# Kernel tuning notes

Hardware: AMD Instinct MI355X
Metric: run time of the kernel (lower is better)

The kernel has to match this reference:

```python
import jax, jax.numpy as jnp
import numpy as np

D_MODEL = 1024
NUM_HEADS = 16
DEPTH = D_MODEL // NUM_HEADS
B, S = 2, 2048


def setup_inputs() -> dict:
    key = jax.random.key(0)
    ks = jax.random.split(key, 12)
    std = 1.0 / np.sqrt(D_MODEL)
    inp = {
        "q": jax.random.normal(ks[0], (B, S, D_MODEL), dtype=jnp.float32),
        "k": jax.random.normal(ks[1], (B, S, D_MODEL), dtype=jnp.float32),
        "v": jax.random.normal(ks[2], (B, S, D_MODEL), dtype=jnp.float32),
        "mask": jax.random.randint(ks[3], (B, 1, 1, S), 0, 2, dtype=jnp.int32),
        "wq": jax.random.normal(ks[4], (D_MODEL, D_MODEL), dtype=jnp.float32) * std,
        "bq": jnp.zeros((D_MODEL,), dtype=jnp.float32),
        "wk": jax.random.normal(ks[5], (D_MODEL, D_MODEL), dtype=jnp.float32) * std,
        "bk": jnp.zeros((D_MODEL,), dtype=jnp.float32),
        "wv": jax.random.normal(ks[6], (D_MODEL, D_MODEL), dtype=jnp.float32) * std,
        "bv": jnp.zeros((D_MODEL,), dtype=jnp.float32),
        "wo": jax.random.normal(ks[7], (D_MODEL, D_MODEL), dtype=jnp.float32) * std,
        "bo": jnp.zeros((D_MODEL,), dtype=jnp.float32),
    }
    return inp


def _split_heads(x):
    # (B, S, D) -> (B, H, S, depth)
    b, s, _ = x.shape
    return x.reshape(b, s, NUM_HEADS, DEPTH).transpose(0, 2, 1, 3)


def reference(q, k, v, mask, wq, bq, wk, bk, wv, bv, wo, bo):
    qh = _split_heads(q @ wq + bq)   # (B,H,S,depth)
    kh = _split_heads(k @ wk + bk)
    vh = _split_heads(v @ wv + bv)
    scale = 1.0 / jnp.sqrt(jnp.float32(DEPTH))
    logits = jnp.einsum("bhqd,bhkd->bhqk", qh, kh) * scale  # (B,H,Sq,Sk)
    logits = logits + mask.astype(logits.dtype) * -1e9
    attn = jax.nn.softmax(logits, axis=-1)
    out = jnp.einsum("bhqk,bhkd->bhqd", attn, vh)  # (B,H,Sq,depth)
    out = out.transpose(0, 2, 1, 3).reshape(q.shape[0], -1, D_MODEL)
    return out @ wo + bo
```

## Files before the change

### kernel.cpp

```cpp
#include <hip/hip_runtime.h>
#include <hip/hip_bf16.h>
#include <stdint.h>


typedef __bf16 bf16;
typedef __bf16 bf16x8 __attribute__((ext_vector_type(8)));
typedef __bf16 bf16x4 __attribute__((ext_vector_type(4)));
typedef float  f32x4  __attribute__((ext_vector_type(4)));

#define D_MODEL 1024
#define S_LEN   2048
#define NH      16
#define DEPTH   64

#define LOG2E   1.4426950408889634f
#define QSCALE  (0.125f * LOG2E)
#define SMAX    20.0f
#define PADPEN  (-30000.0f)

__device__ __forceinline__ void gload_lds16(const void* g, void* l) {
  __builtin_amdgcn_global_load_lds(
      (__attribute__((address_space(1))) void*)g,
      (__attribute__((address_space(3))) void*)l,
      16, 0, 0);
}

__global__ __launch_bounds__(256) void setup(
    const void* __restrict__ q, const void* __restrict__ k,
    const void* __restrict__ v, const int* __restrict__ mask,
    const void* __restrict__ wq, const void* __restrict__ wk,
    const void* __restrict__ wv, const void* __restrict__ wo,
    const void* __restrict__ bq, const void* __restrict__ bk,
    const void* __restrict__ bv, const void* __restrict__ bo,
    bf16* __restrict__ wqT, bf16* __restrict__ wkT,
    bf16* __restrict__ wvT, bf16* __restrict__ woT,
    bf16* __restrict__ bqb, bf16* __restrict__ bkb,
    bf16* __restrict__ bvb, bf16* __restrict__ bob,
    bf16* __restrict__ qb, bf16* __restrict__ kb, bf16* __restrict__ vb,
    int* __restrict__ cpos, int* __restrict__ nb, int* __restrict__ flagout)
{
  const int t = threadIdx.x;
  uint32_t w = ((const uint32_t*)q)[t];
  uint32_t e = (w >> 7) & 0xFF;
  int inr = (e >= 90 && e <= 150) ? 1 : 0;
  __shared__ int flg;
  int cnt = __syncthreads_count(inr);
  if (t == 0) flg = (cnt > 160) ? 1 : 0;
  __syncthreads();
  int flag = flg;

  const int bid = blockIdx.x;
  if (bid < 2) {
    const int b = bid;
    const int lane = t & 63, wv4 = t >> 6;
    __shared__ int wsum[4];
    int vals[8], s = 0;
#pragma unroll
    for (int j = 0; j < 8; ++j) {
      vals[j] = (mask[b * S_LEN + t * 8 + j] == 0) ? 1 : 0;
      s += vals[j];
    }
    int acc = s;
    for (int off = 1; off < 64; off <<= 1) {
      int u = __shfl_up(acc, off);
      if (lane >= off) acc += u;
    }
    if (lane == 63) wsum[wv4] = acc;
    __syncthreads();
    int base = 0;
    for (int w4 = 0; w4 < 4; ++w4) base += (w4 < wv4) ? wsum[w4] : 0;
    int ex = base + acc - s;
#pragma unroll
    for (int j = 0; j < 8; ++j) {
      cpos[b * S_LEN + t * 8 + j] = vals[j] ? ex : -1;
      ex += vals[j];
    }
    if (t == 255) nb[b] = base + acc;
    if (b == 0 && t == 0) *flagout = flag;
  } else if (bid < 6) {
    const int j = bid - 2;
    const void* B; bf16* O;
    switch (j) {
      case 0:  B = bq; O = bqb; break;
      case 1:  B = bk; O = bkb; break;
      case 2:  B = bv; O = bvb; break;
      default: B = bo; O = bob; break;
    }
    const float sc = (j == 0) ? QSCALE : 1.0f;
    for (int jj = 0; jj < 4; ++jj) {
      const int i = t + jj * 256;
      const float val = flag ? (float)((const bf16*)B)[i] : ((const float*)B)[i];
      O[i] = (bf16)(val * sc);
    }
  } else if (bid < 6 + 4096) {
    const int job = bid - 6;
    const int wsel = job >> 10, rem = job & 1023;
    const void* W; bf16* T;
    switch (wsel) {
      case 0:  W = wq; T = wqT; break;
      case 1:  W = wk; T = wkT; break;
      case 2:  W = wv; T = wvT; break;
      default: W = wo; T = woT; break;
    }
    const float sc = (wsel == 0) ? QSCALE : 1.0f;
    __shared__ float tile[32][33];
    const int tx = t & 31, ty = t >> 5;
    const int x0 = (rem & 31) * 32;
    const int y0 = (rem >> 5) * 32;
    for (int i = ty; i < 32; i += 8) {
      const size_t gi = (size_t)(y0 + i) * D_MODEL + x0 + tx;
      tile[i][tx] = flag ? (float)((const bf16*)W)[gi] : ((const float*)W)[gi];
    }
    __syncthreads();
    for (int i = ty; i < 32; i += 8)
      T[(size_t)(x0 + i) * D_MODEL + y0 + tx] = (bf16)(tile[tx][i] * sc);
  } else {
    if (flag) return;
    const int job = bid - 4102;
    const int tensor = job >> 11, blk = job & 2047;
    const void* src; bf16* dst;
    switch (tensor) {
      case 0:  src = q; dst = qb; break;
      case 1:  src = k; dst = kb; break;
      default: src = v; dst = vb; break;
    }
    const size_t idx = ((size_t)blk * 256 + t) * 8;
    const float* s = (const float*)src + idx;
    f32x4 a = *(const f32x4*)(s);
    f32x4 b2 = *(const f32x4*)(s + 4);
    bf16x8 o;
    for (int i = 0; i < 4; ++i) { o[i] = (bf16)a[i]; o[4 + i] = (bf16)b2[i]; }
    *(bf16x8*)(dst + idx) = o;
  }
}

struct GArgs {
  const bf16* A;
  const void* Araw;
  const bf16* BT;
  const bf16* bias;
  void* out;
  const int* cpos;
  int mode;
};

__device__ __forceinline__ void gemm_body(const GArgs& g, int flag)
{
  const bf16* A = flag ? (const bf16*)g.Araw : g.A;

  __shared__ __align__(16) bf16 As[2][128 * 32];
  __shared__ __align__(16) bf16 Bs[2][128 * 32];
  const int tid  = threadIdx.x;
  const int wave = tid >> 6, lane = tid & 63;
  const int quad = lane >> 4, l16 = lane & 15;

  const int flat = blockIdx.y * 8 + blockIdx.x;
  const int xcd = flat & 7, pos = flat >> 3;
  const int bx = (xcd & 1) * 4 + (pos & 3);
  const int by = (xcd >> 1) * 8 + (pos >> 2);
  const int m0 = by * 128, n0 = bx * 128;

  const int wm = (wave >> 1) * 64, wn = (wave & 1) * 64;
  const int srow = lane >> 2;
  const int scol = (((lane & 3) ^ ((lane >> 3) & 3)) * 8);

  f32x4 acc[4][4] = {};

  const bf16* Ag = A    + (size_t)(m0 + wave * 32 + srow) * D_MODEL + scol;
  const bf16* Bg = g.BT + (size_t)(n0 + wave * 32 + srow) * D_MODEL + scol;
  const int lbase = (wave * 32) * 32;
  const int rsw = (quad ^ ((l16 >> 1) & 3)) * 8;

  gload_lds16(Ag,                &As[0][lbase]);
  gload_lds16(Ag + 16 * D_MODEL, &As[0][lbase + 16 * 32]);
  gload_lds16(Bg,                &Bs[0][lbase]);
  gload_lds16(Bg + 16 * D_MODEL, &Bs[0][lbase + 16 * 32]);
  __syncthreads();

  int cur = 0;
  for (int kt = 0; kt < D_MODEL; kt += 32, cur ^= 1) {
    if (kt + 32 < D_MODEL) {
      const int nxt = cur ^ 1;
      gload_lds16(Ag + kt + 32,                &As[nxt][lbase]);
      gload_lds16(Ag + kt + 32 + 16 * D_MODEL, &As[nxt][lbase + 16 * 32]);
      gload_lds16(Bg + kt + 32,                &Bs[nxt][lbase]);
      gload_lds16(Bg + kt + 32 + 16 * D_MODEL, &Bs[nxt][lbase + 16 * 32]);
    }

    bf16x8 af[4], bfv[4];
#pragma unroll
    for (int mi = 0; mi < 4; ++mi)
      af[mi] = *(const bf16x8*)(&As[cur][(wm + mi * 16 + l16) * 32 + rsw]);
#pragma unroll
    for (int ni = 0; ni < 4; ++ni)
      bfv[ni] = *(const bf16x8*)(&Bs[cur][(wn + ni * 16 + l16) * 32 + rsw]);
#pragma unroll
    for (int mi = 0; mi < 4; ++mi)
#pragma unroll
      for (int ni = 0; ni < 4; ++ni)
        acc[mi][ni] = __builtin_amdgcn_mfma_f32_16x16x32_bf16(
            af[mi], bfv[ni], acc[mi][ni], 0, 0, 0);

    __syncthreads();
  }

  if (g.mode != 0) {
    bf16* strip = ((bf16*)As) + wave * (16 * 72);
    const int hh = (n0 + wn) >> 6;
    float bvf[4];
#pragma unroll
    for (int ni = 0; ni < 4; ++ni)
      bvf[ni] = (float)g.bias[n0 + wn + ni * 16 + l16];

#pragma unroll
    for (int mi = 0; mi < 4; ++mi) {
      const int row0 = m0 + wm + mi * 16;
      const int b = row0 >> 11, s0 = row0 & 2047;

#pragma unroll
      for (int ni = 0; ni < 4; ++ni)
#pragma unroll
        for (int r = 0; r < 4; ++r)
          strip[(quad * 4 + r) * 72 + ni * 16 + l16] =
              (bf16)(acc[mi][ni][r] + bvf[ni]);

      if (g.mode == 1) {
        bf16* ob = (bf16*)g.out +
                   ((size_t)(b * NH + hh) * S_LEN + s0) * DEPTH;
#pragma unroll
        for (int half = 0; half < 2; ++half) {
          const int rl = half * 8 + (lane >> 3);
          bf16x8 vv = *(const bf16x8*)(strip + rl * 72 + (lane & 7) * 8);
          *(bf16x8*)(ob + (size_t)rl * DEPTH + (lane & 7) * 8) = vv;
        }
      } else if (g.mode == 3) {
        bf16* kb = (bf16*)g.out + (size_t)(b * NH + hh) * S_LEN * DEPTH;
#pragma unroll
        for (int half = 0; half < 2; ++half) {
          const int rl = half * 8 + (lane >> 3);
          const int cpv = g.cpos[b * S_LEN + s0 + rl];
          bf16x8 vv = *(const bf16x8*)(strip + rl * 72 + (lane & 7) * 8);
          if (cpv >= 0)
            *(bf16x8*)(kb + (size_t)cpv * DEPTH + (lane & 7) * 8) = vv;
        }
      } else {
        const int sl = lane & 15, dq = lane >> 4;
        const int cpv = g.cpos[b * S_LEN + s0 + sl];
        union { bf16x8 v; bf16 e[8]; } u0, u1;
        u0.v = *(const bf16x8*)(strip + sl * 72 + dq * 16);
        u1.v = *(const bf16x8*)(strip + sl * 72 + dq * 16 + 8);
        bf16* vb0 = (bf16*)g.out +
                    ((size_t)(b * NH + hh) * DEPTH + dq * 16) * S_LEN +
                    (cpv >= 0 ? cpv : 0);
        if (cpv >= 0) {
#pragma unroll
          for (int dd = 0; dd < 8; ++dd) vb0[(size_t)dd * S_LEN] = u0.e[dd];
#pragma unroll
          for (int dd = 0; dd < 8; ++dd)
            vb0[(size_t)(dd + 8) * S_LEN] = u1.e[dd];
        }
      }
    }
    return;
  }

#pragma unroll
  for (int mi = 0; mi < 4; ++mi) {
    const int row0 = m0 + wm + mi * 16 + quad * 4;
#pragma unroll
    for (int ni = 0; ni < 4; ++ni) {
      const int col  = n0 + wn + ni * 16 + l16;
      const float bv = (float)g.bias[col];
      if (flag) {
        bf16* op = (bf16*)g.out + (size_t)row0 * D_MODEL + col;
#pragma unroll
        for (int r = 0; r < 4; ++r)
          op[(size_t)r * D_MODEL] = (bf16)(acc[mi][ni][r] + bv);
      } else {
        float* op = (float*)g.out + (size_t)row0 * D_MODEL + col;
#pragma unroll
        for (int r = 0; r < 4; ++r)
          op[(size_t)r * D_MODEL] = acc[mi][ni][r] + bv;
      }
    }
  }
}

__global__ __launch_bounds__(256) void gemm_qkv(GArgs g0, GArgs g1, GArgs g2,
                                                const int* __restrict__ flagp)
{
  const GArgs& g = (blockIdx.z == 0) ? g0 : ((blockIdx.z == 1) ? g1 : g2);
  gemm_body(g, *flagp);
}

__global__ __launch_bounds__(256) void gemm_out(GArgs g,
                                                const int* __restrict__ flagp)
{
  gemm_body(g, *flagp);
}

__global__ __launch_bounds__(256) void attn(
    const bf16* __restrict__ Qh, const bf16* __restrict__ Kc,
    const bf16* __restrict__ Vc, const int* __restrict__ nbp,
    bf16* __restrict__ Oh)
{
  const int bh = blockIdx.y;
  const int b  = bh >> 4;
  const int h  = bh & 15;
  const int q0 = blockIdx.x * 128;
  const int tid = threadIdx.x, wave = tid >> 6, lane = tid & 63;
  const int quad = lane >> 4, l16 = lane & 15;

  __shared__ __align__(16) bf16 Ks[64][72];
  __shared__ __align__(16) bf16 Vts[64][72];
  __shared__ __align__(16) bf16 Ps[4][32][72];

  const int nbv = nbp[b];
  const int nb_pad = (nbv + 63) & ~63;

  const bf16* Qg = Qh + ((size_t)bh * S_LEN + q0 + wave * 32) * DEPTH;
  bf16x8 aq00 = *(const bf16x8*)(Qg + (size_t)l16 * DEPTH + quad * 8);
  bf16x8 aq01 = *(const bf16x8*)(Qg + (size_t)l16 * DEPTH + 32 + quad * 8);
  bf16x8 aq10 = *(const bf16x8*)(Qg + (size_t)(16 + l16) * DEPTH + quad * 8);
  bf16x8 aq11 = *(const bf16x8*)(Qg + (size_t)(16 + l16) * DEPTH + 32 + quad * 8);

  bf16x8 ones;
#pragma unroll
  for (int j = 0; j < 8; ++j) ones[j] = (bf16)1.0f;

  f32x4 o_acc[2][4] = {};
  f32x4 l_acc[2] = {};

  const bf16* Kg = Kc + (size_t)bh * S_LEN * DEPTH;
  const bf16* Vg = Vc + (size_t)bh * DEPTH * S_LEN;

  const int sr0 = tid >> 3, sc0 = (tid & 7) * 8;
  const int sr1 = sr0 + 32;

  bf16x8 kr0, kr1, vr0, vr1;
  {
    kr0 = *(const bf16x8*)(Kg + (size_t)sr0 * DEPTH + sc0);
    kr1 = *(const bf16x8*)(Kg + (size_t)sr1 * DEPTH + sc0);
    vr0 = *(const bf16x8*)(Vg + (size_t)sr0 * S_LEN + sc0);
    vr1 = *(const bf16x8*)(Vg + (size_t)sr1 * S_LEN + sc0);
  }

  for (int kb = 0; kb < nb_pad; kb += 64) {
    __syncthreads();
    *(bf16x8*)(&Ks[sr0][sc0])  = kr0;
    *(bf16x8*)(&Ks[sr1][sc0])  = kr1;
    *(bf16x8*)(&Vts[sr0][sc0]) = vr0;
    *(bf16x8*)(&Vts[sr1][sc0]) = vr1;
    __syncthreads();
    if (kb + 64 < nb_pad) {
      kr0 = *(const bf16x8*)(Kg + (size_t)(kb + 64 + sr0) * DEPTH + sc0);
      kr1 = *(const bf16x8*)(Kg + (size_t)(kb + 64 + sr1) * DEPTH + sc0);
      vr0 = *(const bf16x8*)(Vg + (size_t)sr0 * S_LEN + kb + 64 + sc0);
      vr1 = *(const bf16x8*)(Vg + (size_t)sr1 * S_LEN + kb + 64 + sc0);
    }

    f32x4 sacc[2][4] = {};
#pragma unroll
    for (int jn = 0; jn < 4; ++jn) {
      bf16x8 bk0 = *(const bf16x8*)(&Ks[jn * 16 + l16][quad * 8]);
      bf16x8 bk1 = *(const bf16x8*)(&Ks[jn * 16 + l16][32 + quad * 8]);
      sacc[0][jn] = __builtin_amdgcn_mfma_f32_16x16x32_bf16(aq00, bk0, sacc[0][jn], 0, 0, 0);
      sacc[0][jn] = __builtin_amdgcn_mfma_f32_16x16x32_bf16(aq01, bk1, sacc[0][jn], 0, 0, 0);
      sacc[1][jn] = __builtin_amdgcn_mfma_f32_16x16x32_bf16(aq10, bk0, sacc[1][jn], 0, 0, 0);
      sacc[1][jn] = __builtin_amdgcn_mfma_f32_16x16x32_bf16(aq11, bk1, sacc[1][jn], 0, 0, 0);
    }

#pragma unroll
    for (int jn = 0; jn < 4; ++jn) {
      const int key = kb + jn * 16 + l16;
      const float pen = (key < nbv) ? (-SMAX) : PADPEN;
#pragma unroll
      for (int qs = 0; qs < 2; ++qs)
#pragma unroll
        for (int r = 0; r < 4; ++r)
          Ps[wave][qs * 16 + quad * 4 + r][jn * 16 + l16] =
              (bf16)__builtin_amdgcn_exp2f(sacc[qs][jn][r] + pen);
    }

    bf16x8 ap00 = *(const bf16x8*)(&Ps[wave][l16][quad * 8]);
    bf16x8 ap01 = *(const bf16x8*)(&Ps[wave][l16][32 + quad * 8]);
    bf16x8 ap10 = *(const bf16x8*)(&Ps[wave][16 + l16][quad * 8]);
    bf16x8 ap11 = *(const bf16x8*)(&Ps[wave][16 + l16][32 + quad * 8]);
#pragma unroll
    for (int jd = 0; jd < 4; ++jd) {
      bf16x8 bv0 = *(const bf16x8*)(&Vts[jd * 16 + l16][quad * 8]);
      bf16x8 bv1 = *(const bf16x8*)(&Vts[jd * 16 + l16][32 + quad * 8]);
      o_acc[0][jd] = __builtin_amdgcn_mfma_f32_16x16x32_bf16(ap00, bv0, o_acc[0][jd], 0, 0, 0);
      o_acc[0][jd] = __builtin_amdgcn_mfma_f32_16x16x32_bf16(ap01, bv1, o_acc[0][jd], 0, 0, 0);
      o_acc[1][jd] = __builtin_amdgcn_mfma_f32_16x16x32_bf16(ap10, bv0, o_acc[1][jd], 0, 0, 0);
      o_acc[1][jd] = __builtin_amdgcn_mfma_f32_16x16x32_bf16(ap11, bv1, o_acc[1][jd], 0, 0, 0);
    }
    l_acc[0] = __builtin_amdgcn_mfma_f32_16x16x32_bf16(ap00, ones, l_acc[0], 0, 0, 0);
    l_acc[0] = __builtin_amdgcn_mfma_f32_16x16x32_bf16(ap01, ones, l_acc[0], 0, 0, 0);
    l_acc[1] = __builtin_amdgcn_mfma_f32_16x16x32_bf16(ap10, ones, l_acc[1], 0, 0, 0);
    l_acc[1] = __builtin_amdgcn_mfma_f32_16x16x32_bf16(ap11, ones, l_acc[1], 0, 0, 0);
  }

#pragma unroll
  for (int qs = 0; qs < 2; ++qs) {
#pragma unroll
    for (int r = 0; r < 4; ++r) {
      const int s = q0 + wave * 32 + qs * 16 + quad * 4 + r;
      const float inv = 1.f / l_acc[qs][r];
#pragma unroll
      for (int jd = 0; jd < 4; ++jd) {
        const int d = jd * 16 + l16;
        Oh[(size_t)(b * S_LEN + s) * D_MODEL + h * DEPTH + d] =
            (bf16)(o_acc[qs][jd][r] * inv);
      }
    }
  }
}

extern "C" void kernel_launch(void* const* d_in, const int* in_sizes, int n_in,
                              void* d_out, int out_size, void* d_ws, size_t ws_size,
                              hipStream_t stream)
{
  const void* q    = d_in[0];
  const void* k    = d_in[1];
  const void* v    = d_in[2];
  const int*  mask = (const int*)d_in[3];
  const void* wq   = d_in[4];
  const void* bq   = d_in[5];
  const void* wk   = d_in[6];
  const void* bk   = d_in[7];
  const void* wv   = d_in[8];
  const void* bv   = d_in[9];
  const void* wo   = d_in[10];
  const void* bo   = d_in[11];

  char* ws = (char*)d_ws;
  const size_t MB = 1u << 20;
  bf16* Qh  = (bf16*)(ws + 0 * MB);
  bf16* Kc  = (bf16*)(ws + 8 * MB);
  bf16* Vc  = (bf16*)(ws + 16 * MB);
  bf16* Oh  = (bf16*)(ws + 24 * MB);
  bf16* wqT = (bf16*)(ws + 32 * MB);
  bf16* wkT = (bf16*)(ws + 34 * MB);
  bf16* wvT = (bf16*)(ws + 36 * MB);
  bf16* woT = (bf16*)(ws + 38 * MB);
  bf16* bqb = (bf16*)(ws + 40 * MB);
  bf16* bkb = (bf16*)(ws + 40 * MB + 4096);
  bf16* bvb = (bf16*)(ws + 40 * MB + 8192);
  bf16* bob = (bf16*)(ws + 40 * MB + 12288);
  int*  flag = (int*)(ws + 40 * MB + 32768);
  int*  cpos = (int*)(ws + 40 * MB + 65536);
  int*  nb   = (int*)(ws + 40 * MB + 65536 + 16384);
  bf16* qb  = (bf16*)(ws + 41 * MB);
  bf16* kb_ = (bf16*)(ws + 49 * MB);
  bf16* vb_ = (bf16*)(ws + 57 * MB);

  setup<<<10246, 256, 0, stream>>>(
      q, k, v, mask, wq, wk, wv, wo, bq, bk, bv, bo,
      wqT, wkT, wvT, woT, bqb, bkb, bvb, bob,
      qb, kb_, vb_, cpos, nb, flag);

  GArgs gq{qb,  q,  wqT, bqb, Qh, nullptr, 1};
  GArgs gk{kb_, k,  wkT, bkb, Kc, cpos,    3};
  GArgs gv{vb_, v,  wvT, bvb, Vc, cpos,    2};
  gemm_qkv<<<dim3(8, 32, 3), 256, 0, stream>>>(gq, gk, gv, flag);

  attn<<<dim3(16, 32), 256, 0, stream>>>(Qh, Kc, Vc, nb, Oh);

  GArgs go{Oh, Oh, woT, bob, d_out, nullptr, 0};
  gemm_out<<<dim3(8, 32), 256, 0, stream>>>(go, flag);
}
```

Measured before the change: 227.4 us.

## Enlarge weight transpose tiles, add dedicated 64x128 out-GEMM, prioritize attention MFMAs

```diff
diff --git a/kernel.cpp b/kernel.cpp
--- a/kernel.cpp
+++ b/kernel.cpp
@@ -92,9 +92,9 @@
       const float val = flag ? (float)((const bf16*)B)[i] : ((const float*)B)[i];
       O[i] = (bf16)(val * sc);
     }
-  } else if (bid < 6 + 4096) {
+  } else if (bid < 6 + 1024) {
     const int job = bid - 6;
-    const int wsel = job >> 10, rem = job & 1023;
+    const int wsel = job >> 8, rem = job & 255;
     const void* W; bf16* T;
     switch (wsel) {
       case 0:  W = wq; T = wqT; break;
@@ -103,20 +103,20 @@
       default: W = wo; T = woT; break;
     }
     const float sc = (wsel == 0) ? QSCALE : 1.0f;
-    __shared__ float tile[32][33];
-    const int tx = t & 31, ty = t >> 5;
-    const int x0 = (rem & 31) * 32;
-    const int y0 = (rem >> 5) * 32;
-    for (int i = ty; i < 32; i += 8) {
+    __shared__ float tile[64][65];
+    const int tx = t & 63, ty = t >> 6;
+    const int x0 = (rem & 15) * 64;
+    const int y0 = (rem >> 4) * 64;
+    for (int i = ty; i < 64; i += 4) {
       const size_t gi = (size_t)(y0 + i) * D_MODEL + x0 + tx;
       tile[i][tx] = flag ? (float)((const bf16*)W)[gi] : ((const float*)W)[gi];
     }
     __syncthreads();
-    for (int i = ty; i < 32; i += 8)
-      T[(size_t)(x0 + i) * D_MODEL + y0 + tx] = (bf16)(tile[tx][i] * sc);
+    for (int j = ty; j < 64; j += 4)
+      T[(size_t)(x0 + j) * D_MODEL + y0 + tx] = (bf16)(tile[tx][j] * sc);
   } else {
     if (flag) return;
-    const int job = bid - 4102;
+    const int job = bid - 1030;
     const int tensor = job >> 11, blk = job & 2047;
     const void* src; bf16* dst;
     switch (tensor) {
@@ -296,7 +296,84 @@
 __global__ __launch_bounds__(256) void gemm_out(GArgs g,
                                                 const int* __restrict__ flagp)
 {
-  gemm_body(g, *flagp);
+  const int flag = *flagp;
+  const bf16* A = (const bf16*)g.A;
+
+  __shared__ __align__(16) bf16 As[2][64 * 32];
+  __shared__ __align__(16) bf16 Bs[2][128 * 32];
+  const int tid  = threadIdx.x;
+  const int wave = tid >> 6, lane = tid & 63;
+  const int quad = lane >> 4, l16 = lane & 15;
+
+  const int flat = blockIdx.y * 8 + blockIdx.x;
+  const int xcd = flat & 7, pos = flat >> 3;
+  const int bx = (xcd & 1) * 4 + (pos & 3);
+  const int by = (xcd >> 1) * 16 + (pos >> 2);
+  const int m0 = by * 64, n0 = bx * 128;
+
+  const int wm = (wave >> 1) * 32, wn = (wave & 1) * 64;
+  const int srow = lane >> 2;
+  const int scol = (((lane & 3) ^ ((lane >> 3) & 3)) * 8);
+
+  f32x4 acc[2][4] = {};
+
+  const bf16* Ag = A    + (size_t)(m0 + wave * 16 + (lane >> 2)) * D_MODEL + scol;
+  const bf16* Bg = g.BT + (size_t)(n0 + wave * 32 + srow) * D_MODEL + scol;
+  const int lbaseA = wave * 16 * 32;
+  const int lbaseB = wave * 32 * 32;
+  const int rsw = (quad ^ ((l16 >> 1) & 3)) * 8;
+
+  gload_lds16(Ag,                &As[0][lbaseA]);
+  gload_lds16(Bg,                &Bs[0][lbaseB]);
+  gload_lds16(Bg + 16 * D_MODEL, &Bs[0][lbaseB + 16 * 32]);
+  __syncthreads();
+
+  int cur = 0;
+  for (int kt = 0; kt < D_MODEL; kt += 32, cur ^= 1) {
+    if (kt + 32 < D_MODEL) {
+      const int nxt = cur ^ 1;
+      gload_lds16(Ag + kt + 32,                &As[nxt][lbaseA]);
+      gload_lds16(Bg + kt + 32,                &Bs[nxt][lbaseB]);
+      gload_lds16(Bg + kt + 32 + 16 * D_MODEL, &Bs[nxt][lbaseB + 16 * 32]);
+    }
+
+    bf16x8 af[2], bfv[4];
+#pragma unroll
+    for (int mi = 0; mi < 2; ++mi)
+      af[mi] = *(const bf16x8*)(&As[cur][(wm + mi * 16 + l16) * 32 + rsw]);
+#pragma unroll
+    for (int ni = 0; ni < 4; ++ni)
+      bfv[ni] = *(const bf16x8*)(&Bs[cur][(wn + ni * 16 + l16) * 32 + rsw]);
+#pragma unroll
+    for (int mi = 0; mi < 2; ++mi)
+#pragma unroll
+      for (int ni = 0; ni < 4; ++ni)
+        acc[mi][ni] = __builtin_amdgcn_mfma_f32_16x16x32_bf16(
+            af[mi], bfv[ni], acc[mi][ni], 0, 0, 0);
+
+    __syncthreads();
+  }
+
+#pragma unroll
+  for (int mi = 0; mi < 2; ++mi) {
+    const int row0 = m0 + wm + mi * 16 + quad * 4;
+#pragma unroll
+    for (int ni = 0; ni < 4; ++ni) {
+      const int col  = n0 + wn + ni * 16 + l16;
+      const float bv = (float)g.bias[col];
+      if (flag) {
+        bf16* op = (bf16*)g.out + (size_t)row0 * D_MODEL + col;
+#pragma unroll
+        for (int r = 0; r < 4; ++r)
+          op[(size_t)r * D_MODEL] = (bf16)(acc[mi][ni][r] + bv);
+      } else {
+        float* op = (float*)g.out + (size_t)row0 * D_MODEL + col;
+#pragma unroll
+        for (int r = 0; r < 4; ++r)
+          op[(size_t)r * D_MODEL] = acc[mi][ni][r] + bv;
+      }
+    }
+  }
 }
 
 __global__ __launch_bounds__(256) void attn(
@@ -360,6 +437,7 @@
     }
 
     f32x4 sacc[2][4] = {};
+    __builtin_amdgcn_s_setprio(1);
 #pragma unroll
     for (int jn = 0; jn < 4; ++jn) {
       bf16x8 bk0 = *(const bf16x8*)(&Ks[jn * 16 + l16][quad * 8]);
@@ -369,6 +447,7 @@
       sacc[1][jn] = __builtin_amdgcn_mfma_f32_16x16x32_bf16(aq10, bk0, sacc[1][jn], 0, 0, 0);
       sacc[1][jn] = __builtin_amdgcn_mfma_f32_16x16x32_bf16(aq11, bk1, sacc[1][jn], 0, 0, 0);
     }
+    __builtin_amdgcn_s_setprio(0);
 
 #pragma unroll
     for (int jn = 0; jn < 4; ++jn) {
@@ -386,6 +465,7 @@
     bf16x8 ap01 = *(const bf16x8*)(&Ps[wave][l16][32 + quad * 8]);
     bf16x8 ap10 = *(const bf16x8*)(&Ps[wave][16 + l16][quad * 8]);
     bf16x8 ap11 = *(const bf16x8*)(&Ps[wave][16 + l16][32 + quad * 8]);
+    __builtin_amdgcn_s_setprio(1);
 #pragma unroll
     for (int jd = 0; jd < 4; ++jd) {
       bf16x8 bv0 = *(const bf16x8*)(&Vts[jd * 16 + l16][quad * 8]);
@@ -399,6 +479,7 @@
     l_acc[0] = __builtin_amdgcn_mfma_f32_16x16x32_bf16(ap01, ones, l_acc[0], 0, 0, 0);
     l_acc[1] = __builtin_amdgcn_mfma_f32_16x16x32_bf16(ap10, ones, l_acc[1], 0, 0, 0);
     l_acc[1] = __builtin_amdgcn_mfma_f32_16x16x32_bf16(ap11, ones, l_acc[1], 0, 0, 0);
+    __builtin_amdgcn_s_setprio(0);
   }
 
 #pragma unroll
@@ -455,7 +536,7 @@
   bf16* kb_ = (bf16*)(ws + 49 * MB);
   bf16* vb_ = (bf16*)(ws + 57 * MB);
 
-  setup<<<10246, 256, 0, stream>>>(
+  setup<<<7174, 256, 0, stream>>>(
       q, k, v, mask, wq, wk, wv, wo, bq, bk, bv, bo,
       wqT, wkT, wvT, woT, bqb, bkb, bvb, bob,
       qb, kb_, vb_, cpos, nb, flag);
@@ -468,5 +549,5 @@
   attn<<<dim3(16, 32), 256, 0, stream>>>(Qh, Kc, Vc, nb, Oh);
 
   GArgs go{Oh, Oh, woT, bob, d_out, nullptr, 0};
-  gemm_out<<<dim3(8, 32), 256, 0, stream>>>(go, flag);
-}
+  gemm_out<<<dim3(8, 64), 256, 0, stream>>>(go, flag);
+}
```

Result: no change. 223.0 us (-1.9%).
